# Kernel tuning notes

Measured on AMD Instinct MI355X. Metric: run time of the kernel, lower is better.

The kernel has to match this reference:

```python
import jax, jax.numpy as jnp
import numpy as np
import math

B, R, D = 2048, 512, 256
OUT = 1


def setup_inputs() -> dict:
    key = jax.random.key(0)
    k1, k2, k3, k4 = jax.random.split(key, 4)
    x = jax.random.normal(k1, (B, D), dtype=jnp.float32)
    th = jnp.zeros((R, D), dtype=jnp.float32)
    sign_param = jax.random.normal(k2, (R, D), dtype=jnp.float32) * 0.1
    mask_logit = jnp.full((R, D), -2.0, dtype=jnp.float32)
    log_kappa = jnp.asarray(math.log(6.0), dtype=jnp.float32)
    head_w = jax.random.normal(k3, (OUT, R), dtype=jnp.float32) * (1.0 / np.sqrt(R))
    head_b = jnp.zeros((OUT,), dtype=jnp.float32)
    return {"x": x, "th": th, "sign_param": sign_param,
            "mask_logit": mask_logit, "log_kappa": log_kappa,
            "head_w": head_w, "head_b": head_b}


def _corner_product_z(x, th, sign_param, mask_logit, log_kappa):
    # x: (B, D); th/sign_param/mask_logit: (R, D)
    kappa = jnp.exp(log_kappa)
    sgn = jnp.tanh(sign_param)                 # soft sign in (-1, 1), (R, D)
    # one-sided threshold predicate, broadcast to (B, R, D)
    s = jax.nn.sigmoid(kappa * sgn[None, :, :] * (x[:, None, :] - th[None, :, :]))
    m = jax.nn.sigmoid(mask_logit)             # soft feature mask, (R, D)
    gated = 1.0 - m[None, :, :] * (1.0 - s)    # masked predicate; m->0 => 1 (ignored)
    z = jnp.prod(gated, axis=-1)               # product over features -> (B, R)
    return z, s, m


def reference(x, th, sign_param, mask_logit, log_kappa, head_w, head_b):
    z, _, _ = _corner_product_z(x, th, sign_param, mask_logit, log_kappa)
    y = z @ head_w.T + head_b                  # (B, OUT)
    return y[..., 0] if OUT == 1 else y
```

## Files before the change

### kernel.cpp

```cpp
#include <hip/hip_runtime.h>
#include <math.h>

#define B_TOT 2048
#define R_TOT 512
#define D_TOT 256
#define LOG2E 1.4426950408889634f
#define SCALE_C 2.220446049250313e-16f

typedef float vf4 __attribute__((ext_vector_type(4)));
typedef float vf2 __attribute__((ext_vector_type(2)));


__global__ void prep_kernel(const float* __restrict__ th,
                            const float* __restrict__ sp,
                            const float* __restrict__ ml,
                            const float* __restrict__ lk,
                            float* __restrict__ pp,
                            float* __restrict__ y) {
    int idx = blockIdx.x * 256 + threadIdx.x;
    if (blockIdx.x < (B_TOT / 256)) y[idx] = 0.0f;
    if (idx >= R_TOT * D_TOT) return;
    float kmul = -LOG2E * __builtin_amdgcn_exp2f(lk[0] * LOG2E);
    float u  = sp[idx];
    float eu = __builtin_amdgcn_exp2f(2.0f * LOG2E * u);
    float t  = 1.0f - 2.0f * __builtin_amdgcn_rcpf(eu + 1.0f);
    float A  = kmul * t;
    float Bc = -A * th[idx];
    float em = __builtin_amdgcn_exp2f(LOG2E * ml[idx]);
    float m1 = __builtin_amdgcn_rcpf(1.0f + em);
    int d = idx & 255;
    pp[idx]                       = A;
    pp[R_TOT * D_TOT + idx]       = Bc;
    pp[2 * R_TOT * D_TOT + idx]   = m1 * (((d & 7) == 0) ? SCALE_C : 1.0f);
}

__global__ __launch_bounds__(512, 4) void main_kernel(
        const float* __restrict__ x,
        const float* __restrict__ pp,
        const float* __restrict__ head_w,
        const float* __restrict__ head_b,
        float*       __restrict__ y) {
    __shared__ float rbuf[8][32][36];
    __shared__ float wz[8][32];

    const int tid  = threadIdx.x;
    const int lane = tid & 63;
    const int wave = tid >> 6;
    const int col  = lane & 31;
    const int p    = lane >> 5;
    const int r0   = (blockIdx.x << 3) + wave;
    const int b0   = blockIdx.y << 5;

    const float* ppr = pp + r0 * D_TOT + (col << 3);
    vf4 A0  = *(const vf4*)(ppr);
    vf4 A1  = *(const vf4*)(ppr + 4);
    vf4 Bc0 = *(const vf4*)(ppr + R_TOT * D_TOT);
    vf4 Bc1 = *(const vf4*)(ppr + R_TOT * D_TOT + 4);
    vf4 M0  = *(const vf4*)(ppr + 2 * R_TOT * D_TOT);
    vf4 M1  = *(const vf4*)(ppr + 2 * R_TOT * D_TOT + 4);
    const vf4 Klo = {SCALE_C, 1.0f, 1.0f, 1.0f};

    const float* xb = x + (size_t)(b0 + p) * D_TOT + (col << 3);

    #pragma unroll
    for (int q = 0; q < 8; q++) {
        const float* xq = xb + q * (4 * D_TOT);
        vf4 xa0 = *(const vf4*)(xq);
        vf4 xa1 = *(const vf4*)(xq + 4);
        vf4 xc0 = *(const vf4*)(xq + 2 * D_TOT);
        vf4 xc1 = *(const vf4*)(xq + 2 * D_TOT + 4);

        vf4 ta0 = A0 * xa0 + Bc0;
        vf4 ta1 = A1 * xa1 + Bc1;
        vf4 tc0 = A0 * xc0 + Bc0;
        vf4 tc1 = A1 * xc1 + Bc1;

        vf4 ea0, ea1, ec0, ec1;
        ea0.x = __builtin_amdgcn_exp2f(ta0.x);
        ea0.y = __builtin_amdgcn_exp2f(ta0.y);
        ea0.z = __builtin_amdgcn_exp2f(ta0.z);
        ea0.w = __builtin_amdgcn_exp2f(ta0.w);
        ea1.x = __builtin_amdgcn_exp2f(ta1.x);
        ea1.y = __builtin_amdgcn_exp2f(ta1.y);
        ea1.z = __builtin_amdgcn_exp2f(ta1.z);
        ea1.w = __builtin_amdgcn_exp2f(ta1.w);
        ec0.x = __builtin_amdgcn_exp2f(tc0.x);
        ec0.y = __builtin_amdgcn_exp2f(tc0.y);
        ec0.z = __builtin_amdgcn_exp2f(tc0.z);
        ec0.w = __builtin_amdgcn_exp2f(tc0.w);
        ec1.x = __builtin_amdgcn_exp2f(tc1.x);
        ec1.y = __builtin_amdgcn_exp2f(tc1.y);
        ec1.z = __builtin_amdgcn_exp2f(tc1.z);
        ec1.w = __builtin_amdgcn_exp2f(tc1.w);

        vf4 na0 = M0 * ea0 + Klo;
        vf4 na1 = M1 * ea1 + 1.0f;
        vf4 da0 = ea0 * Klo + Klo;
        vf4 da1 = ea1 + 1.0f;
        vf4 nc0 = M0 * ec0 + Klo;
        vf4 nc1 = M1 * ec1 + 1.0f;
        vf4 dc0 = ec0 * Klo + Klo;
        vf4 dc1 = ec1 + 1.0f;

        vf4 qn_a = na0 * na1;
        vf4 qd_a = da0 * da1;
        vf4 qn_c = nc0 * nc1;
        vf4 qd_c = dc0 * dc1;
        vf2 hn_a = qn_a.lo * qn_a.hi;
        vf2 hd_a = qd_a.lo * qd_a.hi;
        vf2 hn_c = qn_c.lo * qn_c.hi;
        vf2 hd_c = qd_c.lo * qd_c.hi;
        float npA = hn_a.x * hn_a.y;
        float dpA = hd_a.x * hd_a.y;
        float npC = hn_c.x * hn_c.y;
        float dpC = hd_c.x * hd_c.y;

        float inv = __builtin_amdgcn_rcpf(dpA * dpC);
        float rA  = npA * (dpC * inv);
        float rC  = npC * (dpA * inv);
        rbuf[wave][4 * q + p][col]     = rA;
        rbuf[wave][4 * q + 2 + p][col] = rC;
    }

    __syncthreads();

    if (lane < 32) {
        const float* rb2 = &rbuf[wave][lane][0];
        vf4 a0 = *(const vf4*)(rb2)      * *(const vf4*)(rb2 + 4);
        vf4 a1 = *(const vf4*)(rb2 + 8)  * *(const vf4*)(rb2 + 12);
        vf4 a2 = *(const vf4*)(rb2 + 16) * *(const vf4*)(rb2 + 20);
        vf4 a3 = *(const vf4*)(rb2 + 24) * *(const vf4*)(rb2 + 28);
        vf4 m  = (a0 * a1) * (a2 * a3);
        vf2 h  = m.lo * m.hi;
        float z = h.x * h.y;
        wz[wave][lane] = head_w[r0] * z;
    }
    __syncthreads();

    if (wave == 0 && lane < 32) {
        float s = (wz[0][lane] + wz[1][lane]) + (wz[2][lane] + wz[3][lane]);
        float t2 = (wz[4][lane] + wz[5][lane]) + (wz[6][lane] + wz[7][lane]);
        s += t2;
        if (blockIdx.x == 0) s += head_b[0];
        atomicAdd(&y[b0 + lane], s);
    }
}

extern "C" void kernel_launch(void* const* d_in, const int* in_sizes, int n_in,
                              void* d_out, int out_size, void* d_ws, size_t ws_size,
                              hipStream_t stream) {
    const float* x  = (const float*)d_in[0];
    const float* th = (const float*)d_in[1];
    const float* sp = (const float*)d_in[2];
    const float* ml = (const float*)d_in[3];
    const float* lk = (const float*)d_in[4];
    const float* hw = (const float*)d_in[5];
    const float* hb = (const float*)d_in[6];
    float* y = (float*)d_out;

    float* pp = (float*)d_ws;

    prep_kernel<<<R_TOT, 256, 0, stream>>>(th, sp, ml, lk, pp, y);
    dim3 grid(R_TOT / 8, B_TOT / 32, 1);
    main_kernel<<<grid, 512, 0, stream>>>(x, pp, hw, hb, y);
}
```

Measured before the change: 111.5 us.

## Use packed FP32 inline asm and double batch rows per block

The elementwise FMA, mul and add chains in the inner loop are now emitted explicitly as v_pk_fma_f32, v_pk_mul_f32 and v_pk_add_f32 through inline asm. Each block also handles 64 batch rows instead of 32, so the loaded per-rule parameters are reused over twice as many rows and the grid is halved. This cuts VALU instruction count and parameter reloads. In exchange shared memory per block doubles, the unrolled loop is longer and may raise register pressure, and there are fewer blocks to fill the GPU.

```diff
diff --git a/kernel.cpp b/kernel.cpp
--- a/kernel.cpp
+++ b/kernel.cpp
@@ -9,6 +9,34 @@
 
 typedef float vf4 __attribute__((ext_vector_type(4)));
 typedef float vf2 __attribute__((ext_vector_type(2)));
+
+static __device__ __forceinline__ vf2 pk_fma(vf2 a, vf2 b, vf2 c) {
+    vf2 d;
+    asm("v_pk_fma_f32 %0, %1, %2, %3" : "=v"(d) : "v"(a), "v"(b), "v"(c));
+    return d;
+}
+static __device__ __forceinline__ vf2 pk_mul(vf2 a, vf2 b) {
+    vf2 d;
+    asm("v_pk_mul_f32 %0, %1, %2" : "=v"(d) : "v"(a), "v"(b));
+    return d;
+}
+static __device__ __forceinline__ vf2 pk_add(vf2 a, vf2 b) {
+    vf2 d;
+    asm("v_pk_add_f32 %0, %1, %2" : "=v"(d) : "v"(a), "v"(b));
+    return d;
+}
+static __device__ __forceinline__ vf4 pk4_fma(vf4 a, vf4 b, vf4 c) {
+    vf4 d; d.lo = pk_fma(a.lo, b.lo, c.lo); d.hi = pk_fma(a.hi, b.hi, c.hi);
+    return d;
+}
+static __device__ __forceinline__ vf4 pk4_mul(vf4 a, vf4 b) {
+    vf4 d; d.lo = pk_mul(a.lo, b.lo); d.hi = pk_mul(a.hi, b.hi);
+    return d;
+}
+static __device__ __forceinline__ vf4 pk4_add(vf4 a, vf4 b) {
+    vf4 d; d.lo = pk_add(a.lo, b.lo); d.hi = pk_add(a.hi, b.hi);
+    return d;
+}
 
 
 __global__ void prep_kernel(const float* __restrict__ th,
@@ -40,8 +68,8 @@
         const float* __restrict__ head_w,
         const float* __restrict__ head_b,
         float*       __restrict__ y) {
-    __shared__ float rbuf[8][32][36];
-    __shared__ float wz[8][32];
+    __shared__ float rbuf[8][64][36];
+    __shared__ float wz[8][64];
 
     const int tid  = threadIdx.x;
     const int lane = tid & 63;
@@ -49,7 +77,7 @@
     const int col  = lane & 31;
     const int p    = lane >> 5;
     const int r0   = (blockIdx.x << 3) + wave;
-    const int b0   = blockIdx.y << 5;
+    const int b0   = blockIdx.y << 6;
 
     const float* ppr = pp + r0 * D_TOT + (col << 3);
     vf4 A0  = *(const vf4*)(ppr);
@@ -59,21 +87,22 @@
     vf4 M0  = *(const vf4*)(ppr + 2 * R_TOT * D_TOT);
     vf4 M1  = *(const vf4*)(ppr + 2 * R_TOT * D_TOT + 4);
     const vf4 Klo = {SCALE_C, 1.0f, 1.0f, 1.0f};
+    const vf4 One = {1.0f, 1.0f, 1.0f, 1.0f};
 
     const float* xb = x + (size_t)(b0 + p) * D_TOT + (col << 3);
 
     #pragma unroll
-    for (int q = 0; q < 8; q++) {
+    for (int q = 0; q < 16; q++) {
         const float* xq = xb + q * (4 * D_TOT);
         vf4 xa0 = *(const vf4*)(xq);
         vf4 xa1 = *(const vf4*)(xq + 4);
         vf4 xc0 = *(const vf4*)(xq + 2 * D_TOT);
         vf4 xc1 = *(const vf4*)(xq + 2 * D_TOT + 4);
 
-        vf4 ta0 = A0 * xa0 + Bc0;
-        vf4 ta1 = A1 * xa1 + Bc1;
-        vf4 tc0 = A0 * xc0 + Bc0;
-        vf4 tc1 = A1 * xc1 + Bc1;
+        vf4 ta0 = pk4_fma(A0, xa0, Bc0);
+        vf4 ta1 = pk4_fma(A1, xa1, Bc1);
+        vf4 tc0 = pk4_fma(A0, xc0, Bc0);
+        vf4 tc1 = pk4_fma(A1, xc1, Bc1);
 
         vf4 ea0, ea1, ec0, ec1;
         ea0.x = __builtin_amdgcn_exp2f(ta0.x);
@@ -93,23 +122,23 @@
         ec1.z = __builtin_amdgcn_exp2f(tc1.z);
         ec1.w = __builtin_amdgcn_exp2f(tc1.w);
 
-        vf4 na0 = M0 * ea0 + Klo;
-        vf4 na1 = M1 * ea1 + 1.0f;
-        vf4 da0 = ea0 * Klo + Klo;
-        vf4 da1 = ea1 + 1.0f;
-        vf4 nc0 = M0 * ec0 + Klo;
-        vf4 nc1 = M1 * ec1 + 1.0f;
-        vf4 dc0 = ec0 * Klo + Klo;
-        vf4 dc1 = ec1 + 1.0f;
+        vf4 na0 = pk4_fma(M0, ea0, Klo);
+        vf4 na1 = pk4_fma(M1, ea1, One);
+        vf4 da0 = pk4_fma(ea0, Klo, Klo);
+        vf4 da1 = pk4_add(ea1, One);
+        vf4 nc0 = pk4_fma(M0, ec0, Klo);
+        vf4 nc1 = pk4_fma(M1, ec1, One);
+        vf4 dc0 = pk4_fma(ec0, Klo, Klo);
+        vf4 dc1 = pk4_add(ec1, One);
 
-        vf4 qn_a = na0 * na1;
-        vf4 qd_a = da0 * da1;
-        vf4 qn_c = nc0 * nc1;
-        vf4 qd_c = dc0 * dc1;
-        vf2 hn_a = qn_a.lo * qn_a.hi;
-        vf2 hd_a = qd_a.lo * qd_a.hi;
-        vf2 hn_c = qn_c.lo * qn_c.hi;
-        vf2 hd_c = qd_c.lo * qd_c.hi;
+        vf4 qn_a = pk4_mul(na0, na1);
+        vf4 qd_a = pk4_mul(da0, da1);
+        vf4 qn_c = pk4_mul(nc0, nc1);
+        vf4 qd_c = pk4_mul(dc0, dc1);
+        vf2 hn_a = pk_mul(qn_a.lo, qn_a.hi);
+        vf2 hd_a = pk_mul(qd_a.lo, qd_a.hi);
+        vf2 hn_c = pk_mul(qn_c.lo, qn_c.hi);
+        vf2 hd_c = pk_mul(qd_c.lo, qd_c.hi);
         float npA = hn_a.x * hn_a.y;
         float dpA = hd_a.x * hd_a.y;
         float npC = hn_c.x * hn_c.y;
@@ -125,19 +154,23 @@
     __syncthreads();
 
     if (lane < 32) {
-        const float* rb2 = &rbuf[wave][lane][0];
-        vf4 a0 = *(const vf4*)(rb2)      * *(const vf4*)(rb2 + 4);
-        vf4 a1 = *(const vf4*)(rb2 + 8)  * *(const vf4*)(rb2 + 12);
-        vf4 a2 = *(const vf4*)(rb2 + 16) * *(const vf4*)(rb2 + 20);
-        vf4 a3 = *(const vf4*)(rb2 + 24) * *(const vf4*)(rb2 + 28);
-        vf4 m  = (a0 * a1) * (a2 * a3);
-        vf2 h  = m.lo * m.hi;
-        float z = h.x * h.y;
-        wz[wave][lane] = head_w[r0] * z;
+        #pragma unroll
+        for (int h2 = 0; h2 < 2; h2++) {
+            const int row = lane + 32 * h2;
+            const float* rb2 = &rbuf[wave][row][0];
+            vf4 a0 = *(const vf4*)(rb2)      * *(const vf4*)(rb2 + 4);
+            vf4 a1 = *(const vf4*)(rb2 + 8)  * *(const vf4*)(rb2 + 12);
+            vf4 a2 = *(const vf4*)(rb2 + 16) * *(const vf4*)(rb2 + 20);
+            vf4 a3 = *(const vf4*)(rb2 + 24) * *(const vf4*)(rb2 + 28);
+            vf4 m  = (a0 * a1) * (a2 * a3);
+            vf2 h  = m.lo * m.hi;
+            float z = h.x * h.y;
+            wz[wave][row] = head_w[r0] * z;
+        }
     }
     __syncthreads();
 
-    if (wave == 0 && lane < 32) {
+    if (wave == 0) {
         float s = (wz[0][lane] + wz[1][lane]) + (wz[2][lane] + wz[3][lane]);
         float t2 = (wz[4][lane] + wz[5][lane]) + (wz[6][lane] + wz[7][lane]);
         s += t2;
@@ -161,6 +194,6 @@
     float* pp = (float*)d_ws;
 
     prep_kernel<<<R_TOT, 256, 0, stream>>>(th, sp, ml, lk, pp, y);
-    dim3 grid(R_TOT / 8, B_TOT / 32, 1);
+    dim3 grid(R_TOT / 8, B_TOT / 64, 1);
     main_kernel<<<grid, 512, 0, stream>>>(x, pp, hw, hb, y);
 }
```

Result: no change. 112.4 us (+0.8%).

## Process two rules per wave to reuse x loads across rule rows

Applied to the files above, without the earlier changes.

Each block now runs 4 waves instead of 8, and each wave computes two rule rows (r and r+4) from the same x vectors. This halves the global loads of x per rule and makes use of all threads in the reduction stage. The cost is more registers per thread, since two rules' parameters are held, and fewer threads per block, which may reduce latency hiding.

```diff
diff --git a/kernel.cpp b/kernel.cpp
--- a/kernel.cpp
+++ b/kernel.cpp
@@ -34,7 +34,63 @@
     pp[2 * R_TOT * D_TOT + idx]   = m1 * (((d & 7) == 0) ? SCALE_C : 1.0f);
 }
 
-__global__ __launch_bounds__(512, 4) void main_kernel(
+struct R2 { float rA, rC; };
+static __device__ __forceinline__ R2 rule_body(
+        vf4 A0, vf4 A1, vf4 Bc0, vf4 Bc1, vf4 M0, vf4 M1, vf4 Klo,
+        vf4 xa0, vf4 xa1, vf4 xc0, vf4 xc1) {
+    vf4 ta0 = A0 * xa0 + Bc0;
+    vf4 ta1 = A1 * xa1 + Bc1;
+    vf4 tc0 = A0 * xc0 + Bc0;
+    vf4 tc1 = A1 * xc1 + Bc1;
+
+    vf4 ea0, ea1, ec0, ec1;
+    ea0.x = __builtin_amdgcn_exp2f(ta0.x);
+    ea0.y = __builtin_amdgcn_exp2f(ta0.y);
+    ea0.z = __builtin_amdgcn_exp2f(ta0.z);
+    ea0.w = __builtin_amdgcn_exp2f(ta0.w);
+    ea1.x = __builtin_amdgcn_exp2f(ta1.x);
+    ea1.y = __builtin_amdgcn_exp2f(ta1.y);
+    ea1.z = __builtin_amdgcn_exp2f(ta1.z);
+    ea1.w = __builtin_amdgcn_exp2f(ta1.w);
+    ec0.x = __builtin_amdgcn_exp2f(tc0.x);
+    ec0.y = __builtin_amdgcn_exp2f(tc0.y);
+    ec0.z = __builtin_amdgcn_exp2f(tc0.z);
+    ec0.w = __builtin_amdgcn_exp2f(tc0.w);
+    ec1.x = __builtin_amdgcn_exp2f(tc1.x);
+    ec1.y = __builtin_amdgcn_exp2f(tc1.y);
+    ec1.z = __builtin_amdgcn_exp2f(tc1.z);
+    ec1.w = __builtin_amdgcn_exp2f(tc1.w);
+
+    vf4 na0 = M0 * ea0 + Klo;
+    vf4 na1 = M1 * ea1 + 1.0f;
+    vf4 da0 = ea0 * Klo + Klo;
+    vf4 da1 = ea1 + 1.0f;
+    vf4 nc0 = M0 * ec0 + Klo;
+    vf4 nc1 = M1 * ec1 + 1.0f;
+    vf4 dc0 = ec0 * Klo + Klo;
+    vf4 dc1 = ec1 + 1.0f;
+
+    vf4 qn_a = na0 * na1;
+    vf4 qd_a = da0 * da1;
+    vf4 qn_c = nc0 * nc1;
+    vf4 qd_c = dc0 * dc1;
+    vf2 hn_a = qn_a.lo * qn_a.hi;
+    vf2 hd_a = qd_a.lo * qd_a.hi;
+    vf2 hn_c = qn_c.lo * qn_c.hi;
+    vf2 hd_c = qd_c.lo * qd_c.hi;
+    float npA = hn_a.x * hn_a.y;
+    float dpA = hd_a.x * hd_a.y;
+    float npC = hn_c.x * hn_c.y;
+    float dpC = hd_c.x * hd_c.y;
+
+    float inv = __builtin_amdgcn_rcpf(dpA * dpC);
+    R2 out;
+    out.rA = npA * (dpC * inv);
+    out.rC = npC * (dpA * inv);
+    return out;
+}
+
+__global__ __launch_bounds__(256, 4) void main_kernel(
         const float* __restrict__ x,
         const float* __restrict__ pp,
         const float* __restrict__ head_w,
@@ -48,16 +104,24 @@
     const int wave = tid >> 6;
     const int col  = lane & 31;
     const int p    = lane >> 5;
-    const int r0   = (blockIdx.x << 3) + wave;
+    const int rA0  = (blockIdx.x << 3) + wave;
+    const int rB0  = rA0 + 4;
     const int b0   = blockIdx.y << 5;
 
-    const float* ppr = pp + r0 * D_TOT + (col << 3);
-    vf4 A0  = *(const vf4*)(ppr);
-    vf4 A1  = *(const vf4*)(ppr + 4);
-    vf4 Bc0 = *(const vf4*)(ppr + R_TOT * D_TOT);
-    vf4 Bc1 = *(const vf4*)(ppr + R_TOT * D_TOT + 4);
-    vf4 M0  = *(const vf4*)(ppr + 2 * R_TOT * D_TOT);
-    vf4 M1  = *(const vf4*)(ppr + 2 * R_TOT * D_TOT + 4);
+    const float* pa = pp + rA0 * D_TOT + (col << 3);
+    vf4 Aa0  = *(const vf4*)(pa);
+    vf4 Aa1  = *(const vf4*)(pa + 4);
+    vf4 Ba0  = *(const vf4*)(pa + R_TOT * D_TOT);
+    vf4 Ba1  = *(const vf4*)(pa + R_TOT * D_TOT + 4);
+    vf4 Ma0  = *(const vf4*)(pa + 2 * R_TOT * D_TOT);
+    vf4 Ma1  = *(const vf4*)(pa + 2 * R_TOT * D_TOT + 4);
+    const float* pb = pp + rB0 * D_TOT + (col << 3);
+    vf4 Ab0  = *(const vf4*)(pb);
+    vf4 Ab1  = *(const vf4*)(pb + 4);
+    vf4 Bb0  = *(const vf4*)(pb + R_TOT * D_TOT);
+    vf4 Bb1  = *(const vf4*)(pb + R_TOT * D_TOT + 4);
+    vf4 Mb0  = *(const vf4*)(pb + 2 * R_TOT * D_TOT);
+    vf4 Mb1  = *(const vf4*)(pb + 2 * R_TOT * D_TOT + 4);
     const vf4 Klo = {SCALE_C, 1.0f, 1.0f, 1.0f};
 
     const float* xb = x + (size_t)(b0 + p) * D_TOT + (col << 3);
@@ -70,62 +134,23 @@
         vf4 xc0 = *(const vf4*)(xq + 2 * D_TOT);
         vf4 xc1 = *(const vf4*)(xq + 2 * D_TOT + 4);
 
-        vf4 ta0 = A0 * xa0 + Bc0;
-        vf4 ta1 = A1 * xa1 + Bc1;
-        vf4 tc0 = A0 * xc0 + Bc0;
-        vf4 tc1 = A1 * xc1 + Bc1;
+        R2 ra = rule_body(Aa0, Aa1, Ba0, Ba1, Ma0, Ma1, Klo,
+                          xa0, xa1, xc0, xc1);
+        R2 rb = rule_body(Ab0, Ab1, Bb0, Bb1, Mb0, Mb1, Klo,
+                          xa0, xa1, xc0, xc1);
 
-        vf4 ea0, ea1, ec0, ec1;
-        ea0.x = __builtin_amdgcn_exp2f(ta0.x);
-        ea0.y = __builtin_amdgcn_exp2f(ta0.y);
-        ea0.z = __builtin_amdgcn_exp2f(ta0.z);
-        ea0.w = __builtin_amdgcn_exp2f(ta0.w);
-        ea1.x = __builtin_amdgcn_exp2f(ta1.x);
-        ea1.y = __builtin_amdgcn_exp2f(ta1.y);
-        ea1.z = __builtin_amdgcn_exp2f(ta1.z);
-        ea1.w = __builtin_amdgcn_exp2f(ta1.w);
-        ec0.x = __builtin_amdgcn_exp2f(tc0.x);
-        ec0.y = __builtin_amdgcn_exp2f(tc0.y);
-        ec0.z = __builtin_amdgcn_exp2f(tc0.z);
-        ec0.w = __builtin_amdgcn_exp2f(tc0.w);
-        ec1.x = __builtin_amdgcn_exp2f(tc1.x);
-        ec1.y = __builtin_amdgcn_exp2f(tc1.y);
-        ec1.z = __builtin_amdgcn_exp2f(tc1.z);
-        ec1.w = __builtin_amdgcn_exp2f(tc1.w);
-
-        vf4 na0 = M0 * ea0 + Klo;
-        vf4 na1 = M1 * ea1 + 1.0f;
-        vf4 da0 = ea0 * Klo + Klo;
-        vf4 da1 = ea1 + 1.0f;
-        vf4 nc0 = M0 * ec0 + Klo;
-        vf4 nc1 = M1 * ec1 + 1.0f;
-        vf4 dc0 = ec0 * Klo + Klo;
-        vf4 dc1 = ec1 + 1.0f;
-
-        vf4 qn_a = na0 * na1;
-        vf4 qd_a = da0 * da1;
-        vf4 qn_c = nc0 * nc1;
-        vf4 qd_c = dc0 * dc1;
-        vf2 hn_a = qn_a.lo * qn_a.hi;
-        vf2 hd_a = qd_a.lo * qd_a.hi;
-        vf2 hn_c = qn_c.lo * qn_c.hi;
-        vf2 hd_c = qd_c.lo * qd_c.hi;
-        float npA = hn_a.x * hn_a.y;
-        float dpA = hd_a.x * hd_a.y;
-        float npC = hn_c.x * hn_c.y;
-        float dpC = hd_c.x * hd_c.y;
-
-        float inv = __builtin_amdgcn_rcpf(dpA * dpC);
-        float rA  = npA * (dpC * inv);
-        float rC  = npC * (dpA * inv);
-        rbuf[wave][4 * q + p][col]     = rA;
-        rbuf[wave][4 * q + 2 + p][col] = rC;
+        rbuf[wave][4 * q + p][col]         = ra.rA;
+        rbuf[wave][4 * q + 2 + p][col]     = ra.rC;
+        rbuf[wave + 4][4 * q + p][col]     = rb.rA;
+        rbuf[wave + 4][4 * q + 2 + p][col] = rb.rC;
     }
 
     __syncthreads();
 
-    if (lane < 32) {
-        const float* rb2 = &rbuf[wave][lane][0];
+    {
+        const int slot = tid >> 5;
+        const int bb   = tid & 31;
+        const float* rb2 = &rbuf[slot][bb][0];
         vf4 a0 = *(const vf4*)(rb2)      * *(const vf4*)(rb2 + 4);
         vf4 a1 = *(const vf4*)(rb2 + 8)  * *(const vf4*)(rb2 + 12);
         vf4 a2 = *(const vf4*)(rb2 + 16) * *(const vf4*)(rb2 + 20);
@@ -133,12 +158,12 @@
         vf4 m  = (a0 * a1) * (a2 * a3);
         vf2 h  = m.lo * m.hi;
         float z = h.x * h.y;
-        wz[wave][lane] = head_w[r0] * z;
+        wz[slot][bb] = head_w[(blockIdx.x << 3) + slot] * z;
     }
     __syncthreads();
 
     if (wave == 0 && lane < 32) {
-        float s = (wz[0][lane] + wz[1][lane]) + (wz[2][lane] + wz[3][lane]);
+        float s  = (wz[0][lane] + wz[1][lane]) + (wz[2][lane] + wz[3][lane]);
         float t2 = (wz[4][lane] + wz[5][lane]) + (wz[6][lane] + wz[7][lane]);
         s += t2;
         if (blockIdx.x == 0) s += head_b[0];
@@ -162,5 +187,5 @@
 
     prep_kernel<<<R_TOT, 256, 0, stream>>>(th, sp, ml, lk, pp, y);
     dim3 grid(R_TOT / 8, B_TOT / 32, 1);
-    main_kernel<<<grid, 512, 0, stream>>>(x, pp, hw, hb, y);
+    main_kernel<<<grid, 256, 0, stream>>>(x, pp, hw, hb, y);
 }
```

After: 107.0 us. 4.0% less time.
